# Kernel tuning notes

Hardware: AMD Instinct MI355X
Metric: run time of the kernel (lower is better)

## Reference

```python
import jax, jax.numpy as jnp
import numpy as np

EPS = 1e-6
TEMPERATURE = 1.0

def _rms_norm(x):
    fp = x.astype(jnp.float32)
    inv = jax.lax.rsqrt(jnp.mean(fp * fp, axis=-1, keepdims=True) + EPS)
    return (fp * inv).astype(x.dtype)

def setup_inputs() -> dict:
    key = jax.random.key(0)
    k1, k2, k3 = jax.random.split(key, 3)
    n, b, t, h = 8, 4, 2048, 2048
    num_sources = 12
    values = jax.random.normal(k1, (n, b, t, h), dtype=jnp.float32)
    w_query = jax.random.normal(k2, (num_sources, h), dtype=jnp.float32) * 0.02
    key_pos_bias = jax.random.normal(k3, (num_sources, h), dtype=jnp.float32) * 0.02
    return {"values": values, "w_query": w_query, "key_pos_bias": key_pos_bias, "position": n}

def reference(values, w_query, key_pos_bias, position):
    # values: [n, b, t, h] with n == position
    keys = _rms_norm(values)
    bias = key_pos_bias[:position].astype(keys.dtype)          # [n, h]
    keys = keys + bias[:, None, None, :]
    query = w_query[position].astype(keys.dtype)               # [h]
    scale = np.sqrt(values.shape[-1]) * TEMPERATURE
    scores = jnp.einsum('h,nbth->nbt', query, keys) / scale    # [n, b, t]
    alpha = jax.nn.softmax(scores.astype(jnp.float32), axis=0).astype(values.dtype)
    routed = jnp.einsum('nbt,nbth->bth', alpha, values)        # [b, t, h]
    return routed, jnp.transpose(alpha, (1, 2, 0))
```

## Files before the change

### kernel.cpp

```cpp
#include <hip/hip_runtime.h>
#include <math.h>

#define N 8
#define B 4
#define T 2048
#define H 2048

static constexpr float EPS = 1e-6f;
static constexpr float INV_SCALE = 1.0f / 45.25483399593904f;

typedef float floatx4 __attribute__((ext_vector_type(4)));

__global__ __launch_bounds__(256) void qb_kernel(
    const float* __restrict__ w_query,
    const float* __restrict__ key_pos_bias,
    const int* __restrict__ position,
    float* __restrict__ qb ) {
    const int pos = *position;
    const float* q = w_query + (size_t)pos * H;
    const int tid = threadIdx.x;
    float part[N];
#pragma unroll
    for (int n = 0; n < N; ++n) part[n] = 0.f;
    for (int h = tid; h < H; h += 256) {
        const float qv = q[h];
#pragma unroll
        for (int n = 0; n < N; ++n)
            part[n] += qv * key_pos_bias[(size_t)n * H + h];
    }
#pragma unroll
    for (int n = 0; n < N; ++n) {
#pragma unroll
        for (int off = 32; off; off >>= 1)
            part[n] += __shfl_xor(part[n], off);
    }
    __shared__ float red[4][N];
    const int wave = tid >> 6, lane = tid & 63;
    if (lane == 0) {
#pragma unroll
        for (int n = 0; n < N; ++n) red[wave][n] = part[n];
    }
    __syncthreads();
    if (tid < N)
        qb[tid] = red[0][tid] + red[1][tid] + red[2][tid] + red[3][tid];
}

__global__ __launch_bounds__(512, 6) void router_kernel(
    const float* __restrict__ values,
    const float* __restrict__ w_query,
    const int* __restrict__ position,
    const float* __restrict__ qb,
    float* __restrict__ routed,
    float* __restrict__ alpha_out) {
    const int tid = threadIdx.x;
    const int bt  = blockIdx.x;
    const int b   = bt >> 11;
    const int t   = bt & (T - 1);
    const int h0  = tid * 4;

    const int pos = *position;
    const floatx4 q = *(const floatx4*)(w_query + (size_t)pos * H + h0);

    const float* vbase = values + ((size_t)b * T + t) * H + h0;
    const size_t nstride = (size_t)B * T * H;

    floatx4 v[N];
    float ss[N], qd[N];
#pragma unroll
    for (int n = 0; n < N; ++n) {
        const floatx4 a = __builtin_nontemporal_load(
            (const floatx4*)(vbase + (size_t)n * nstride));
        v[n] = a;
        ss[n] = a.x*a.x + a.y*a.y + a.z*a.z + a.w*a.w;
        qd[n] = q.x*a.x + q.y*a.y + q.z*a.z + q.w*a.w;
    }

#pragma unroll
    for (int n = 0; n < N; ++n) {
#pragma unroll
        for (int off = 32; off; off >>= 1) {
            ss[n] += __shfl_xor(ss[n], off);
            qd[n] += __shfl_xor(qd[n], off);
        }
    }

    __shared__ float red[8][2 * N];
    __shared__ float tot[2 * N];
    const int wave = tid >> 6, lane = tid & 63;
    if (lane == 0) {
#pragma unroll
        for (int n = 0; n < N; ++n) {
            red[wave][n]     = ss[n];
            red[wave][N + n] = qd[n];
        }
    }
    __syncthreads();
    if (tid < 2 * N) {
        float s = 0.f;
#pragma unroll
        for (int w = 0; w < 8; ++w) s += red[w][tid];
        tot[tid] = s;
    }
    __syncthreads();

    float sc[N];
    float m = -INFINITY;
#pragma unroll
    for (int n = 0; n < N; ++n) {
        const float inv = rsqrtf(tot[n] * (1.0f / (float)H) + EPS);
        sc[n] = (inv * tot[N + n] + qb[n]) * INV_SCALE;
        m = fmaxf(m, sc[n]);
    }
    float ssum = 0.f;
    float alpha[N];
#pragma unroll
    for (int n = 0; n < N; ++n) {
        alpha[n] = __expf(sc[n] - m);
        ssum += alpha[n];
    }
    const float rs = 1.0f / ssum;
#pragma unroll
    for (int n = 0; n < N; ++n) alpha[n] *= rs;

    floatx4 o;
    o.x = 0.f; o.y = 0.f; o.z = 0.f; o.w = 0.f;
#pragma unroll
    for (int n = 0; n < N; ++n) {
        o.x += alpha[n] * v[n].x;
        o.y += alpha[n] * v[n].y;
        o.z += alpha[n] * v[n].z;
        o.w += alpha[n] * v[n].w;
    }
    __builtin_nontemporal_store(o, (floatx4*)(routed + ((size_t)b * T + t) * H + h0));

    if (tid == 0) {
        float* ap = alpha_out + ((size_t)b * T + t) * N;
        floatx4 a0 = { alpha[0], alpha[1], alpha[2], alpha[3] };
        floatx4 a1 = { alpha[4], alpha[5], alpha[6], alpha[7] };
        *(floatx4*)(ap)     = a0;
        *(floatx4*)(ap + 4) = a1;
    }
}

extern "C" void kernel_launch(void* const* d_in, const int* in_sizes, int n_in,
                              void* d_out, int out_size, void* d_ws, size_t ws_size,
                              hipStream_t stream) {
    const float* values   = (const float*)d_in[0];
    const float* w_query  = (const float*)d_in[1];
    const float* bias     = (const float*)d_in[2];
    const int*   position = (const int*)d_in[3];
    float* out = (float*)d_out;
    float* qb  = (float*)d_ws;

    qb_kernel<<<1, 256, 0, stream>>>(w_query, bias, position, qb);
    router_kernel<<<B * T, 512, 0, stream>>>(
        values, w_query, position, qb,
        out, out + (size_t)B * T * H);
}
```

Baseline: 684.0 us.

## Replace per-row shuffle reductions with shared-memory transpose reduction

The router kernel now writes each thread's per-source partial sums (sum of squares and query dot) into a shared-memory array. Each wave then reduces one source across all threads, which replaces the 16 separate 6-step shuffle reductions with 2 reductions per wave. The qb kernel is also rewritten to use vectorized 8-wide loads. The cost is about 36KB of shared memory per block, which may limit occupancy given the 6-blocks launch bound, plus extra LDS traffic that may cause bank conflicts.

```diff
diff --git a/kernel.cpp b/kernel.cpp
--- a/kernel.cpp
+++ b/kernel.cpp
@@ -5,11 +5,13 @@
 #define B 4
 #define T 2048
 #define H 2048
+#define THREADS 512
 
 static constexpr float EPS = 1e-6f;
 static constexpr float INV_SCALE = 1.0f / 45.25483399593904f;
 
 typedef float floatx4 __attribute__((ext_vector_type(4)));
+typedef float floatx2 __attribute__((ext_vector_type(2)));
 
 __global__ __launch_bounds__(256) void qb_kernel(
     const float* __restrict__ w_query,
@@ -17,16 +19,20 @@
     const int* __restrict__ position,
     float* __restrict__ qb ) {
     const int pos = *position;
-    const float* q = w_query + (size_t)pos * H;
     const int tid = threadIdx.x;
+    const int h0  = tid * 8;
+    const float* qp = w_query + (size_t)pos * H + h0;
+    const floatx4 q0 = *(const floatx4*)(qp);
+    const floatx4 q1 = *(const floatx4*)(qp + 4);
+
     float part[N];
 #pragma unroll
-    for (int n = 0; n < N; ++n) part[n] = 0.f;
-    for (int h = tid; h < H; h += 256) {
-        const float qv = q[h];
-#pragma unroll
-        for (int n = 0; n < N; ++n)
-            part[n] += qv * key_pos_bias[(size_t)n * H + h];
+    for (int n = 0; n < N; ++n) {
+        const float* bp = key_pos_bias + (size_t)n * H + h0;
+        const floatx4 b0 = *(const floatx4*)(bp);
+        const floatx4 b1 = *(const floatx4*)(bp + 4);
+        part[n] = q0.x*b0.x + q0.y*b0.y + q0.z*b0.z + q0.w*b0.w
+                + q1.x*b1.x + q1.y*b1.y + q1.z*b1.z + q1.w*b1.w;
     }
 #pragma unroll
     for (int n = 0; n < N; ++n) {
@@ -45,7 +51,7 @@
         qb[tid] = red[0][tid] + red[1][tid] + red[2][tid] + red[3][tid];
 }
 
-__global__ __launch_bounds__(512, 6) void router_kernel(
+__global__ __launch_bounds__(THREADS, 6) void router_kernel(
     const float* __restrict__ values,
     const float* __restrict__ w_query,
     const int* __restrict__ position,
@@ -64,42 +70,38 @@
     const float* vbase = values + ((size_t)b * T + t) * H + h0;
     const size_t nstride = (size_t)B * T * H;
 
+    __shared__ float part[THREADS][18];
+    __shared__ float tot[2 * N];
+
     floatx4 v[N];
-    float ss[N], qd[N];
 #pragma unroll
     for (int n = 0; n < N; ++n) {
         const floatx4 a = __builtin_nontemporal_load(
             (const floatx4*)(vbase + (size_t)n * nstride));
         v[n] = a;
-        ss[n] = a.x*a.x + a.y*a.y + a.z*a.z + a.w*a.w;
-        qd[n] = q.x*a.x + q.y*a.y + q.z*a.z + q.w*a.w;
+        const float ss = a.x*a.x + a.y*a.y + a.z*a.z + a.w*a.w;
+        const float qd = q.x*a.x + q.y*a.y + q.z*a.z + q.w*a.w;
+        *(floatx2*)&part[tid][2 * n] = floatx2{ss, qd};
     }
+    __syncthreads();
 
+    const int wave = tid >> 6, lane = tid & 63;
+    {
+        float ssum = 0.f, qsum = 0.f;
 #pragma unroll
-    for (int n = 0; n < N; ++n) {
+        for (int k = 0; k < 8; ++k) {
+            const floatx2 p = *(const floatx2*)&part[lane + 64 * k][2 * wave];
+            ssum += p.x; qsum += p.y;
+        }
 #pragma unroll
         for (int off = 32; off; off >>= 1) {
-            ss[n] += __shfl_xor(ss[n], off);
-            qd[n] += __shfl_xor(qd[n], off);
+            ssum += __shfl_xor(ssum, off);
+            qsum += __shfl_xor(qsum, off);
         }
-    }
-
-    __shared__ float red[8][2 * N];
-    __shared__ float tot[2 * N];
-    const int wave = tid >> 6, lane = tid & 63;
-    if (lane == 0) {
-#pragma unroll
-        for (int n = 0; n < N; ++n) {
-            red[wave][n]     = ss[n];
-            red[wave][N + n] = qd[n];
+        if (lane == 0) {
+            tot[wave]     = ssum;
+            tot[N + wave] = qsum;
         }
-    }
-    __syncthreads();
-    if (tid < 2 * N) {
-        float s = 0.f;
-#pragma unroll
-        for (int w = 0; w < 8; ++w) s += red[w][tid];
-        tot[tid] = s;
     }
     __syncthreads();
 
@@ -153,7 +155,7 @@
     float* qb  = (float*)d_ws;
 
     qb_kernel<<<1, 256, 0, stream>>>(w_query, bias, position, qb);
-    router_kernel<<<B * T, 512, 0, stream>>>(
+    router_kernel<<<B * T, THREADS, 0, stream>>>(
         values, w_query, position, qb,
         out, out + (size_t)B * T * H);
 }
```

New measurement: 677.4 us. Within noise of the previous version (-1.0%).
